# Optimization experiments

Measured on AMD Instinct MI355X. Metric: run time of the kernel, lower is better.

The kernel has to match this reference:

```python
import jax, jax.numpy as jnp
import numpy as np

BS, T, G, C = 64, 128, 36, 256
H = 256          # gaze LSTM hidden
P = 256          # spatial projected size
PT = 256         # temporal projected size
Q = 16           # queue size
NC = 10          # num classes
NEG = -1e9


def setup_inputs() -> dict:
    key = jax.random.key(0)
    ks = jax.random.split(key, 40)
    s = 0.02
    D = C + H
    inp = {
        'cnn_feat_seq': jax.random.normal(ks[0], (BS, T, G, C), jnp.float32),
        'gaze_seq': jax.random.normal(ks[1], (BS, T, 3), jnp.float32),
        # init-hidden / init-cell MLPs (Linear(3,H), Tanh, Linear(H,H), Tanh)
        'init_h_w1': jax.random.normal(ks[2], (H, 3)) * s, 'init_h_b1': jnp.zeros((H,)),
        'init_h_w2': jax.random.normal(ks[3], (H, H)) * s, 'init_h_b2': jnp.zeros((H,)),
        'init_c_w1': jax.random.normal(ks[4], (H, 3)) * s, 'init_c_b1': jnp.zeros((H,)),
        'init_c_w2': jax.random.normal(ks[5], (H, H)) * s, 'init_c_b2': jnp.zeros((H,)),
        # LSTM (input 3, hidden H), torch gate order i,f,g,o
        'lstm_wih': jax.random.normal(ks[6], (4 * H, 3)) * s, 'lstm_whh': jax.random.normal(ks[7], (4 * H, H)) * s,
        'lstm_bih': jnp.zeros((4 * H,)), 'lstm_bhh': jnp.zeros((4 * H,)),
        # spatial attention
        'sa_wl': jax.random.normal(ks[8], (P, H)) * s, 'sa_bl': jnp.zeros((P,)),
        'sa_wc': jax.random.normal(ks[9], (P, C)) * s, 'sa_bc': jnp.zeros((P,)),
        'sa_wz': jax.random.normal(ks[10], (P,)) * s,
        # temporal attention
        'ta_wl': jax.random.normal(ks[11], (PT, H)) * s, 'ta_bl': jnp.zeros((PT,)),
        'ta_wv': jax.random.normal(ks[12], (PT, C)) * s, 'ta_bv': jnp.zeros((PT,)),
        'ta_wz': jax.random.normal(ks[13], (PT,)) * s,
        # MLP classifier: Linear(D,D) -> Linear(D,D) -> Linear(D,NC), no nonlinearity
        'mlp_w1': jax.random.normal(ks[14], (D, D)) * s, 'mlp_b1': jnp.zeros((D,)),
        'mlp_w2': jax.random.normal(ks[15], (D, D)) * s, 'mlp_b2': jnp.zeros((D,)),
        'mlp_w3': jax.random.normal(ks[16], (NC, D)) * s, 'mlp_b3': jnp.zeros((NC,)),
    }
    return inp


def _forward(cnn_feat_seq, gaze_seq,
             init_h_w1, init_h_b1, init_h_w2, init_h_b2,
             init_c_w1, init_c_b1, init_c_w2, init_c_b2,
             lstm_wih, lstm_whh, lstm_bih, lstm_bhh,
             sa_wl, sa_bl, sa_wc, sa_bc, sa_wz,
             ta_wl, ta_bl, ta_wv, ta_bv, ta_wz,
             mlp_w1, mlp_b1, mlp_w2, mlp_b2, mlp_w3, mlp_b3):
    bs, num_frame = gaze_seq.shape[0], gaze_seq.shape[1]
    mean_gaze = jnp.mean(gaze_seq, axis=1)  # (bs, 3)
    # init MLP ends with Tanh, and forward applies F.tanh again
    h0 = jnp.tanh(jnp.tanh(jnp.tanh(mean_gaze @ init_h_w1.T + init_h_b1) @ init_h_w2.T + init_h_b2))
    c0 = jnp.tanh(jnp.tanh(jnp.tanh(mean_gaze @ init_c_w1.T + init_c_b1) @ init_c_w2.T + init_c_b2))
    buf_s0 = jnp.zeros((Q, bs, C), cnn_feat_seq.dtype)
    buf_h0 = jnp.zeros((Q, bs, H), cnn_feat_seq.dtype)
    qidx = jnp.arange(Q)

    def step(carry, xs):
        h, c, buf_s, buf_h, i = carry
        feat, gaze = xs  # (bs,G,C), (bs,3)
        # --- spatial additive attention over grids ---
        Hp = h @ sa_wl.T + sa_bl                                  # (bs,P)
        Vp = jnp.einsum('bgc,pc->bgp', feat, sa_wc) + sa_bc       # (bs,G,P)
        zs = jnp.tanh(Hp[:, None, :] + Vp) @ sa_wz                # (bs,G)
        sw = jax.nn.softmax(zs, axis=1)
        spat = jnp.einsum('bgc,bg->bc', feat, sw)                 # (bs,C)
        # --- rolling queues (newest last) ---
        buf_s = jnp.concatenate([buf_s[1:], spat[None]], axis=0)
        buf_h = jnp.concatenate([buf_h[1:], h[None]], axis=0)
        count = jnp.minimum(i + 1, Q)
        mask = qidx >= (Q - count)                                # (Q,) valid slots
        # --- temporal additive attention over queue ---
        Hq = jnp.einsum('qbh,ph->qbp', buf_h, ta_wl) + ta_bl
        Vq = jnp.einsum('qbc,pc->qbp', buf_s, ta_wv) + ta_bv
        zt = jnp.tanh(Hq + Vq) @ ta_wz                            # (Q,bs)
        zt = jnp.where(mask[:, None], zt, NEG)
        tw = jax.nn.softmax(zt, axis=0)
        temp = jnp.einsum('qbc,qb->bc', buf_s, tw)                # (bs,C)
        # --- one LSTM step on gaze ---
        gates = gaze @ lstm_wih.T + lstm_bih + h @ lstm_whh.T + lstm_bhh
        gi, gf, gg, go = jnp.split(gates, 4, axis=-1)
        c = jax.nn.sigmoid(gf) * c + jax.nn.sigmoid(gi) * jnp.tanh(gg)
        h = jax.nn.sigmoid(go) * jnp.tanh(c)
        # --- classifier on concat(temporal_feat, lstm_hidden) ---
        fc = jnp.concatenate([temp, h], axis=1)                   # (bs, C+H)
        pred = ((fc @ mlp_w1.T + mlp_b1) @ mlp_w2.T + mlp_b2) @ mlp_w3.T + mlp_b3
        return (h, c, buf_s, buf_h, i + 1), pred

    feats_t = jnp.swapaxes(cnn_feat_seq, 0, 1)  # (T,bs,G,C)
    gaze_t = jnp.swapaxes(gaze_seq, 0, 1)       # (T,bs,3)
    _, preds = jax.lax.scan(step, (h0, c0, buf_s0, buf_h0, jnp.int32(0)), (feats_t, gaze_t))
    # torch cats (1,bs,NC) pieces along dim=1 -> (1, T*bs, NC)
    return preds.reshape(1, num_frame * bs, NC)


def reference(cnn_feat_seq, gaze_seq,
              init_h_w1, init_h_b1, init_h_w2, init_h_b2,
              init_c_w1, init_c_b1, init_c_w2, init_c_b2,
              lstm_wih, lstm_whh, lstm_bih, lstm_bhh,
              sa_wl, sa_bl, sa_wc, sa_bc, sa_wz,
              ta_wl, ta_bl, ta_wv, ta_bv, ta_wz,
              mlp_w1, mlp_b1, mlp_w2, mlp_b2, mlp_w3, mlp_b3):
    return _forward(cnn_feat_seq, gaze_seq,
                    init_h_w1, init_h_b1, init_h_w2, init_h_b2,
                    init_c_w1, init_c_b1, init_c_w2, init_c_b2,
                    lstm_wih, lstm_whh, lstm_bih, lstm_bhh,
                    sa_wl, sa_bl, sa_wc, sa_bc, sa_wz,
                    ta_wl, ta_bl, ta_wv, ta_bv, ta_wz,
                    mlp_w1, mlp_b1, mlp_w2, mlp_b2, mlp_w3, mlp_b3)
```

## Files before the change

kernel.cpp:

```cpp
#include <hip/hip_runtime.h>
#include <cstdint>
#include <cstddef>

#define BSZ 64
#define TT  128
#define GG  36
#define CC  256
#define HH  256
#define QQ  16
#define NCLS 10
#define NROW 8192
#define SP_ROWS 32

using short8  = __attribute__((ext_vector_type(8))) short;
using f32x4   = __attribute__((ext_vector_type(4))) float;
using half2_t = __attribute__((ext_vector_type(2))) _Float16;
typedef unsigned int u32;
typedef unsigned short u16;

#define OFF_WI    0u
#define OFF_WF    131072u
#define OFF_WG    262144u
#define OFF_WO    393216u
#define OFF_SAWL  524288u
#define OFF_TAWL  655360u
#define OFF_TAWV  786432u
#define OFF_SAWC  917504u
#define OFF_W32   1048576u
#define OFF_WC    1069056u
#define OFF_BC    1089536u
#define OFF_H0F16 1089792u
#define OFF_C0    1122560u
#define OFF_HSEQ  1188096u
#define OFF_HSEQB 9642240u
#define OFF_HPSA  13869312u
#define OFF_HQ    22257920u
#define OFF_SPAT  30646528u
#define OFF_SPATB 39035136u
#define OFF_ZSC   43229440u
#define WS_NEEDED 43262208u

__device__ __forceinline__ float rcp_fast(float x){
#if __has_builtin(__builtin_amdgcn_rcpf)
  return __builtin_amdgcn_rcpf(x);
#else
  return 1.f/x;
#endif
}
__device__ __forceinline__ float fast_sig(float x){ return rcp_fast(1.f+__expf(-x)); }
__device__ __forceinline__ float fast_tanh(float x){ float e=__expf(2.f*x); return 1.f-2.f*rcp_fast(e+1.f); }
__device__ __forceinline__ u16 f2bf(float f){
  u32 u = __builtin_bit_cast(u32, f);
  u += 0x7fffu + ((u>>16)&1u);
  return (u16)(u>>16);
}
__device__ __forceinline__ float bf2f(u16 b){
  u32 u = ((u32)b)<<16; return __builtin_bit_cast(float, u);
}
__device__ __forceinline__ u32 cvtpk_bf16(float a, float b){
  u32 p;
  asm("v_cvt_pk_bf16_f32 %0, %1, %2" : "=v"(p) : "v"(a), "v"(b));
  return p;
}
__device__ __forceinline__ u32 packf16(float a, float b){
  half2_t h; h.x = (_Float16)a; h.y = (_Float16)b;
  return __builtin_bit_cast(u32, h);
}
__device__ __forceinline__ float dot2(u32 w, u32 h, float acc){
#if __has_builtin(__builtin_amdgcn_fdot2)
  return __builtin_amdgcn_fdot2(__builtin_bit_cast(half2_t, w),
                                __builtin_bit_cast(half2_t, h), acc, false);
#else
  half2_t a = __builtin_bit_cast(half2_t, w), b = __builtin_bit_cast(half2_t, h);
  return acc + (float)a.x*(float)b.x + (float)a.y*(float)b.y;
#endif
}
__device__ __forceinline__ f32x4 mfma16(short8 a, short8 b, f32x4 c){
  return __builtin_amdgcn_mfma_f32_16x16x32_bf16(a, b, c, 0, 0, 0);
}

__global__ void __launch_bounds__(256) k_prep1(const float* __restrict__ whh,
    const float* __restrict__ sawl, const float* __restrict__ tawl,
    const float* __restrict__ tawv, const float* __restrict__ sawc,
    const float* __restrict__ w3, const float* __restrict__ w2, char* ws){
  int blk = blockIdx.x, tid = threadIdx.x;
  if (blk < 512){
    u32* wq = (u32*)ws;
    for (int rr = 0; rr < 2; ++rr){
      int row = blk*2 + rr;
      float v  = whh[row*256 + tid];
      float vn = __shfl_down(v, 1);
      if ((tid & 1) == 0){
        int typ = row >> 8;
        int j   = row & 255;
        wq[typ*32768 + (tid>>1)*256 + j] = packf16(v, vn);
      }
    }
  } else if (blk < 544){
    int rel = blk - 512;
    int mat = rel >> 3;
    const float* src; u16* dst;
    if (mat==0){ src=sawl; dst=(u16*)(ws+OFF_SAWL); }
    else if (mat==1){ src=tawl; dst=(u16*)(ws+OFF_TAWL); }
    else if (mat==2){ src=tawv; dst=(u16*)(ws+OFF_TAWV); }
    else { src=sawc; dst=(u16*)(ws+OFF_SAWC); }
    int base = (rel & 7)*8192 + tid;
    if (mat < 3){
      for (int i = 0; i < 32; ++i){ int e = base + i*256; dst[e] = f2bf(src[e]); }
    } else {
      for (int i = 0; i < 32; ++i){
        int e = base + i*256;
        int col = e >> 8, kk = e & 255;
        dst[col*256 + (kk ^ ((col&7)<<3))] = f2bf(src[e]);
      }
    }
  } else {
    int idx = (blk-544)*256 + tid;
    int o = idx >> 9, k2 = idx & 511;
    float acc = 0.f;
    for (int m = 0; m < 512; ++m) acc = fmaf(w3[o*512+m], w2[m*512+k2], acc);
    ((float*)(ws+OFF_W32))[idx] = acc;
  }
}

__global__ void __launch_bounds__(256) k_prep2(const float* __restrict__ w1,
    const float* __restrict__ b1, const float* __restrict__ w3,
    const float* __restrict__ b2, const float* __restrict__ b3,
    const float* __restrict__ gaze,
    const float* __restrict__ ihw1, const float* __restrict__ ihb1,
    const float* __restrict__ ihw2, const float* __restrict__ ihb2,
    const float* __restrict__ icw1, const float* __restrict__ icb1,
    const float* __restrict__ icw2, const float* __restrict__ icb2,
    char* ws){
  int blk = blockIdx.x, tid = threadIdx.x;
  const float* W32 = (const float*)(ws+OFF_W32);
  if (blk < 20){
    int idx = blk*256 + tid; int o = idx>>9, k = idx&511;
    float acc = 0.f;
    for (int m = 0; m < 512; ++m) acc = fmaf(W32[o*512+m], w1[m*512+k], acc);
    ((float*)(ws+OFF_WC))[idx] = acc;
  } else if (blk == 20){
    if (tid < 10){
      float acc = b3[tid];
      for (int m = 0; m < 512; ++m) acc = fmaf(W32[tid*512+m], b1[m], acc);
      for (int m = 0; m < 512; ++m) acc = fmaf(w3[tid*512+m], b2[m], acc);
      ((float*)(ws+OFF_BC))[tid] = acc;
    }
  } else {
    int b = blk - 21;
    __shared__ float red0[128], red1[128], red2[128];
    __shared__ float mg[3];
    __shared__ float x1[256];
    if (tid < 128){
      const float* gp = gaze + b*384 + tid*3;
      red0[tid] = gp[0]; red1[tid] = gp[1]; red2[tid] = gp[2];
    }
    __syncthreads();
    for (int s = 64; s >= 1; s >>= 1){
      if (tid < s){ red0[tid]+=red0[tid+s]; red1[tid]+=red1[tid+s]; red2[tid]+=red2[tid+s]; }
      __syncthreads();
    }
    if (tid == 0){ mg[0]=red0[0]*(1.f/128.f); mg[1]=red1[0]*(1.f/128.f); mg[2]=red2[0]*(1.f/128.f); }
    __syncthreads();
    for (int which = 0; which < 2; ++which){
      const float* aw1 = which? icw1 : ihw1; const float* ab1 = which? icb1 : ihb1;
      const float* aw2 = which? icw2 : ihw2; const float* ab2 = which? icb2 : ihb2;
      float v = fast_tanh(fmaf(aw1[tid*3+2],mg[2], fmaf(aw1[tid*3+1],mg[1], fmaf(aw1[tid*3],mg[0], ab1[tid]))));
      x1[tid] = v;
      __syncthreads();
      float acc = ab2[tid];
      for (int k = 0; k < 256; ++k) acc = fmaf(aw2[tid*256+k], x1[k], acc);
      float h0 = fast_tanh(fast_tanh(acc));
      if (which == 0){
        float* hseq = (float*)(ws+OFF_HSEQ);
        hseq[(size_t)(0*64 + b)*256 + tid] = h0;
        float hn = __shfl_down(h0, 1);
        if ((tid&1)==0){
          ((u32*)(ws+OFF_HSEQB))[((size_t)(0*64+b)*256 + tid)>>1] = ((u32)f2bf(hn)<<16) | f2bf(h0);
          ((u32*)(ws+OFF_H0F16))[b*128 + (tid>>1)] = packf16(h0, hn);
        }
      } else {
        ((float*)(ws+OFF_C0))[b*256 + tid] = h0;
      }
      __syncthreads();
    }
  }
}

__global__ void __launch_bounds__(256) k_gates(const float* __restrict__ gaze,
    const float* __restrict__ wih, const float* __restrict__ bih,
    const float* __restrict__ bhh, char* ws){
  int b = blockIdx.x, tq = blockIdx.y, j = threadIdx.x;
  u32* pIG = (u32*)(ws+OFF_HPSA);
  u32* pFO = (u32*)(ws+OFF_HQ);
  float bi = bih[j]     + bhh[j];
  float bf_= bih[256+j] + bhh[256+j];
  float bg = bih[512+j] + bhh[512+j];
  float bo = bih[768+j] + bhh[768+j];
  float ui0=wih[j*3],       ui1=wih[j*3+1],       ui2=wih[j*3+2];
  float uf0=wih[(256+j)*3], uf1=wih[(256+j)*3+1], uf2=wih[(256+j)*3+2];
  float ug0=wih[(512+j)*3], ug1=wih[(512+j)*3+1], ug2=wih[(512+j)*3+2];
  float uo0=wih[(768+j)*3], uo1=wih[(768+j)*3+1], uo2=wih[(768+j)*3+2];
#pragma unroll
  for (int dt = 0; dt < 4; ++dt){
    int t = tq*4 + dt;
    float g0 = gaze[b*384 + t*3], g1 = gaze[b*384 + t*3 + 1], g2 = gaze[b*384 + t*3 + 2];
    float aI = fmaf(ui2,g2, fmaf(ui1,g1, fmaf(ui0,g0, bi)));
    float aF = fmaf(uf2,g2, fmaf(uf1,g1, fmaf(uf0,g0, bf_)));
    float aG = fmaf(ug2,g2, fmaf(ug1,g1, fmaf(ug0,g0, bg)));
    float aO = fmaf(uo2,g2, fmaf(uo1,g1, fmaf(uo0,g0, bo)));
    size_t idx = (size_t)(b*128 + t)*256 + j;
    pIG[idx] = packf16(aI, aG);
    pFO[idx] = packf16(aF, aO);
  }
}

__global__ void __launch_bounds__(512, 2) k_lstm(char* ws){
  int b = blockIdx.x, tid = threadIdx.x;
  int half = tid >> 8;
  int j = tid & 255;
  __shared__ __align__(16) uint4 lds_w4[4*512];
  __shared__ __align__(16) u32 hbuf[2][128];
  __shared__ float p_lds[256];

  const u32* wq = (const u32*)ws;
  const u32* wA = wq + (half ? 1 : 0) * 32768;
  const u32* wB = wq + (half ? 3 : 2) * 32768;
  u32 w0[128], w1r[112];
#pragma unroll
  for (int c = 0; c < 128; ++c) w0[c] = wA[c*256 + j];
#pragma unroll
  for (int c = 0; c < 112; ++c) w1r[c] = wB[c*256 + j];
#pragma unroll
  for (int cq = 0; cq < 4; ++cq){
    uint4 wv;
    wv.x = wB[(112 + cq*4 + 0)*256 + j];
    wv.y = wB[(112 + cq*4 + 1)*256 + j];
    wv.z = wB[(112 + cq*4 + 2)*256 + j];
    wv.w = wB[(112 + cq*4 + 3)*256 + j];
    lds_w4[cq*512 + tid] = wv;
  }
  if (tid < 128) hbuf[0][tid] = ((const u32*)(ws+OFF_H0F16))[b*128 + tid];
  float creg = half ? ((const float*)(ws+OFF_C0))[b*256 + j] : 0.f;

  const u32* gin = (const u32*)(ws + (half ? OFF_HQ : OFF_HPSA)) + (size_t)b*128*256 + j;
  float* hseq = (float*)(ws+OFF_HSEQ);
  u32* hseqb = (u32*)(ws+OFF_HSEQB);
  float hv_prev = 0.f; u32 hpk_prev = 0;
  u32 gcur = gin[0];
  __syncthreads();

  for (int t = 0; t < 128; ++t){
    int cur = t & 1, nxt = cur ^ 1;
    if (half == 1 && t > 0){
      hseq[((size_t)t*64 + b)*256 + j] = hv_prev;
      if ((j & 1) == 0)
        hseqb[(((size_t)t*64 + b)*256 + j)>>1] = hpk_prev;
    }
    u32 gnext = 0;
    if (t < 127) gnext = gin[(size_t)(t+1)*256];
    uint4 wp[4];
#pragma unroll
    for (int cq = 0; cq < 4; ++cq) wp[cq] = lds_w4[cq*512 + tid];

    half2_t gh = __builtin_bit_cast(half2_t, gcur);
    float aA0 = (float)gh.x, aA1 = 0.f;
    float aB0 = (float)gh.y, aB1 = 0.f;
#pragma unroll
    for (int c4 = 0; c4 < 28; ++c4){
      uint4 h4 = *reinterpret_cast<const uint4*>(&hbuf[cur][c4*4]);
      aA0 = dot2(w0[c4*4+0], h4.x, aA0); aB0 = dot2(w1r[c4*4+0], h4.x, aB0);
      aA1 = dot2(w0[c4*4+1], h4.y, aA1); aB1 = dot2(w1r[c4*4+1], h4.y, aB1);
      aA0 = dot2(w0[c4*4+2], h4.z, aA0); aB0 = dot2(w1r[c4*4+2], h4.z, aB0);
      aA1 = dot2(w0[c4*4+3], h4.w, aA1); aB1 = dot2(w1r[c4*4+3], h4.w, aB1);
    }
#pragma unroll
    for (int cq = 0; cq < 4; ++cq){
      int c4 = 28 + cq;
      uint4 h4 = *reinterpret_cast<const uint4*>(&hbuf[cur][c4*4]);
      uint4 wv = wp[cq];
      aA0 = dot2(w0[c4*4+0], h4.x, aA0); aB0 = dot2(wv.x, h4.x, aB0);
      aA1 = dot2(w0[c4*4+1], h4.y, aA1); aB1 = dot2(wv.y, h4.y, aB1);
      aA0 = dot2(w0[c4*4+2], h4.z, aA0); aB0 = dot2(wv.z, h4.z, aB0);
      aA1 = dot2(w0[c4*4+3], h4.w, aA1); aB1 = dot2(wv.w, h4.w, aB1);
    }
    float aA = aA0 + aA1, aB = aB0 + aB1;
    if (half == 0){
      p_lds[j] = fast_sig(aA) * fast_tanh(aB);
    }
    __syncthreads();
    if (half == 1){
      float p = p_lds[j];
      creg = fmaf(fast_sig(aA), creg, p);
      float hv = fast_sig(aB) * fast_tanh(creg);
      float hn = __shfl_down(hv, 1);
      if ((j & 1) == 0) hbuf[nxt][j>>1] = packf16(hv, hn);
      hv_prev = hv;
      hpk_prev = ((u32)f2bf(hn)<<16) | f2bf(hv);
    }
    __syncthreads();
    gcur = gnext;
  }
  if (half == 1){
    hseq[((size_t)128*64 + b)*256 + j] = hv_prev;
    if ((j & 1) == 0)
      hseqb[(((size_t)128*64 + b)*256 + j)>>1] = hpk_prev;
  }
}

__global__ void __launch_bounds__(256) k_proj1(const float* __restrict__ sabl,
    const float* __restrict__ sabc, const float* __restrict__ tabl,
    const float* __restrict__ tabv, char* ws){
  int bx = blockIdx.x, which = blockIdx.y;
  const u16* A = (const u16*)(ws+OFF_HSEQB);
  const u16* B = (const u16*)(ws + (which? OFF_TAWL : OFF_SAWL));
  float* Out   = (float*)(ws + (which? OFF_HQ : OFF_HPSA));
  const float* bp1 = which? tabl : sabl;
  const float* bp2 = which? tabv : sabc;
  int tid = threadIdx.x, w = tid>>6, l = tid&63;
  int lr = l&15, lk = l>>4;
  int rb = bx*64;
  short8 afr[4][8];
#pragma unroll
  for (int m = 0; m < 4; ++m)
#pragma unroll
    for (int k = 0; k < 8; ++k)
      afr[m][k] = *(const short8*)(const void*)(A + (size_t)(rb + m*16 + lr)*256 + k*32 + lk*8);
#pragma unroll
  for (int n = 0; n < 4; ++n){
    int cb = w*64 + n*16;
    int col = cb + lr;
    float bias = bp1[col] + bp2[col];
    f32x4 a0 = {0.f,0.f,0.f,0.f}, a1 = a0, a2 = a0, a3 = a0;
#pragma unroll
    for (int k = 0; k < 8; ++k){
      short8 bf = *(const short8*)(const void*)(B + (size_t)col*256 + k*32 + lk*8);
      a0 = mfma16(afr[0][k], bf, a0);
      a1 = mfma16(afr[1][k], bf, a1);
      a2 = mfma16(afr[2][k], bf, a2);
      a3 = mfma16(afr[3][k], bf, a3);
    }
#pragma unroll
    for (int q = 0; q < 4; ++q){
      Out[(size_t)(rb + 0*16 + lk*4 + q)*256 + col] = a0[q] + bias;
      Out[(size_t)(rb + 1*16 + lk*4 + q)*256 + col] = a1[q] + bias;
      Out[(size_t)(rb + 2*16 + lk*4 + q)*256 + col] = a2[q] + bias;
      Out[(size_t)(rb + 3*16 + lk*4 + q)*256 + col] = a3[q] + bias;
    }
  }
}

__global__ void __launch_bounds__(512, 2) k_spatial(const float* __restrict__ feat,
    const float* __restrict__ sawz, char* ws){
  __shared__ __align__(16) u16 featb[48*256];
  __shared__ __align__(16) float hp[256];
  __shared__ float wzs[256];
  __shared__ float zsbuf[8][48];
  __shared__ float swl[36];
  __shared__ float psum[2][256];
  int bx = blockIdx.x, tid = threadIdx.x, w = tid>>6, l = tid&63;
  int lr = l&15, lk = l>>4;
  int colbase = w*32;
  const float* hpsa = (const float*)(ws+OFF_HPSA);
  const u16* Bw = (const u16*)(ws+OFF_SAWC);

  short8 breg[2][8];
#pragma unroll
  for (int n = 0; n < 2; ++n){
    int col = colbase + n*16 + lr;
#pragma unroll
    for (int k = 0; k < 8; ++k)
      breg[n][k] = *(const short8*)(const void*)(Bw + (size_t)col*256 + ((k*32 + lk*8) ^ ((col&7)<<3)));
  }
  if (tid < 256) wzs[tid] = sawz[tid];

  float4 pf[5]; float4 ph;
  {
    int r0 = bx*SP_ROWS;
    int t = r0>>6, b = r0&63;
    const float4* fb = (const float4*)(feat + ((size_t)(b*128 + t))*9216);
#pragma unroll
    for (int ii = 0; ii < 4; ++ii) pf[ii] = fb[tid + ii*512];
    if (tid < 256) pf[4] = fb[2048 + tid];
    if (tid < 64) ph = ((const float4*)(hpsa + (size_t)r0*256))[tid];
  }
  __syncthreads();

  for (int i = 0; i < SP_ROWS; ++i){
    int r = bx*SP_ROWS + i;
#pragma unroll
    for (int ii = 0; ii < 4; ++ii){
      int e = tid + ii*512;
      int g = e >> 6, c4 = e & 63;
      uint2 pp;
      pp.x = cvtpk_bf16(pf[ii].x, pf[ii].y);
      pp.y = cvtpk_bf16(pf[ii].z, pf[ii].w);
      *reinterpret_cast<uint2*>((u32*)featb + g*128 + ((c4*2) ^ ((g&7)<<2))) = pp;
    }
    if (tid < 256){
      int e = 2048 + tid;
      int g = e >> 6, c4 = e & 63;
      uint2 pp;
      pp.x = cvtpk_bf16(pf[4].x, pf[4].y);
      pp.y = cvtpk_bf16(pf[4].z, pf[4].w);
      *reinterpret_cast<uint2*>((u32*)featb + g*128 + ((c4*2) ^ ((g&7)<<2))) = pp;
    }
    if (tid < 64) *reinterpret_cast<float4*>(hp + tid*4) = ph;
    __syncthreads();
    if (i + 1 < SP_ROWS){
      int rn = r + 1;
      int t = rn>>6, b = rn&63;
      const float4* fb = (const float4*)(feat + ((size_t)(b*128 + t))*9216);
#pragma unroll
      for (int ii = 0; ii < 4; ++ii) pf[ii] = fb[tid + ii*512];
      if (tid < 256) pf[4] = fb[2048 + tid];
      if (tid < 64) ph = ((const float4*)(hpsa + (size_t)rn*256))[tid];
    }
    float zacc[3][4] = {{0.f}};
#pragma unroll
    for (int m = 0; m < 3; ++m){
      short8 afr[8];
#pragma unroll
      for (int k = 0; k < 8; ++k){
        int g = m*16 + lr;
        afr[k] = *(const short8*)(const void*)(featb + g*256 + ((k*32 + lk*8) ^ ((g&7)<<3)));
      }
#pragma unroll
      for (int n = 0; n < 2; ++n){
        f32x4 a = {0.f,0.f,0.f,0.f};
#pragma unroll
        for (int k = 0; k < 8; ++k) a = mfma16(afr[k], breg[n][k], a);
        int col = colbase + n*16 + lr;
        float hpl = hp[col], wzv = wzs[col];
#pragma unroll
        for (int q = 0; q < 4; ++q)
          zacc[m][q] += fast_tanh(a[q] + hpl)*wzv;
      }
    }
#pragma unroll
    for (int m = 0; m < 3; ++m)
#pragma unroll
      for (int q = 0; q < 4; ++q){
        float v = zacc[m][q];
        v += __shfl_xor(v, 1); v += __shfl_xor(v, 2);
        v += __shfl_xor(v, 4); v += __shfl_xor(v, 8);
        if (lr == 0) zsbuf[w][m*16 + lk*4 + q] = v;
      }
    __syncthreads();
    if (w == 0){
      float z = -1e30f;
      if (l < 36)
        z = zsbuf[0][l]+zsbuf[1][l]+zsbuf[2][l]+zsbuf[3][l]
          + zsbuf[4][l]+zsbuf[5][l]+zsbuf[6][l]+zsbuf[7][l];
      float mx = z;
      for (int d = 1; d < 64; d <<= 1) mx = fmaxf(mx, __shfl_xor(mx, d));
      float e = (l < 36)? __expf(z - mx) : 0.f;
      float s = e;
      for (int d = 1; d < 64; d <<= 1) s += __shfl_xor(s, d);
      if (l < 36) swl[l] = e * rcp_fast(s);
    }
    __syncthreads();
    {
      int hsel = tid >> 8, col = tid & 255;
      float part = 0.f;
#pragma unroll
      for (int gg = 0; gg < 18; ++gg){
        int g = hsel*18 + gg;
        part = fmaf(swl[g], bf2f(featb[g*256 + (col ^ ((g&7)<<3))]), part);
      }
      psum[hsel][col] = part;
    }
    __syncthreads();
    if (tid < 256){
      float acc = psum[0][tid] + psum[1][tid];
      ((float*)(ws+OFF_SPAT))[(size_t)r*256 + tid] = acc;
      float an = __shfl_down(acc, 1);
      if ((tid & 1) == 0)
        ((u32*)(ws+OFF_SPATB))[((size_t)r*256 + tid)>>1] = cvtpk_bf16(acc, an);
    }
  }
}

__global__ void __launch_bounds__(256) k_proj2(const float* __restrict__ tawz, char* ws){
  int bx = blockIdx.x;
  int tid = threadIdx.x, w = tid>>6, l = tid&63;
  int lr = l&15, lk = l>>4;
  int rb = bx*64;
  const u16* A = (const u16*)(ws+OFF_SPATB);
  const u16* B = (const u16*)(ws+OFF_TAWV);
  const float* Hq = (const float*)(ws+OFF_HQ);
  __shared__ float zbuf[4][64];
  short8 afr[4][8];
#pragma unroll
  for (int m = 0; m < 4; ++m)
#pragma unroll
    for (int k = 0; k < 8; ++k)
      afr[m][k] = *(const short8*)(const void*)(A + (size_t)(rb + m*16 + lr)*256 + k*32 + lk*8);
  float racc[4][4] = {{0.f}};
#pragma unroll
  for (int n = 0; n < 4; ++n){
    int col = w*64 + n*16 + lr;
    float tzl = tawz[col];
    f32x4 a0 = {0.f,0.f,0.f,0.f}, a1 = a0, a2 = a0, a3 = a0;
#pragma unroll
    for (int k = 0; k < 8; ++k){
      short8 bf = *(const short8*)(const void*)(B + (size_t)col*256 + k*32 + lk*8);
      a0 = mfma16(afr[0][k], bf, a0);
      a1 = mfma16(afr[1][k], bf, a1);
      a2 = mfma16(afr[2][k], bf, a2);
      a3 = mfma16(afr[3][k], bf, a3);
    }
#pragma unroll
    for (int q = 0; q < 4; ++q){
      racc[0][q] += fast_tanh(a0[q] + Hq[(size_t)(rb + 0*16 + lk*4 + q)*256 + col]) * tzl;
      racc[1][q] += fast_tanh(a1[q] + Hq[(size_t)(rb + 1*16 + lk*4 + q)*256 + col]) * tzl;
      racc[2][q] += fast_tanh(a2[q] + Hq[(size_t)(rb + 2*16 + lk*4 + q)*256 + col]) * tzl;
      racc[3][q] += fast_tanh(a3[q] + Hq[(size_t)(rb + 3*16 + lk*4 + q)*256 + col]) * tzl;
    }
  }
#pragma unroll
  for (int m = 0; m < 4; ++m)
#pragma unroll
    for (int q = 0; q < 4; ++q){
      float v = racc[m][q];
      v += __shfl_xor(v, 1); v += __shfl_xor(v, 2);
      v += __shfl_xor(v, 4); v += __shfl_xor(v, 8);
      if (lr == 0) zbuf[w][m*16 + lk*4 + q] = v;
    }
  __syncthreads();
  if (tid < 64)
    ((float*)(ws+OFF_ZSC))[rb + tid] = zbuf[0][tid]+zbuf[1][tid]+zbuf[2][tid]+zbuf[3][tid];
}

__global__ void __launch_bounds__(256) k_final(float* __restrict__ out, char* ws){
  int bx = blockIdx.x;
  int b = bx & 63, tb = bx >> 6;
  int t0 = tb*8;
  int tid = threadIdx.x;
  int wv = tid>>6, l = tid&63;
  __shared__ float spw[23][256];
  __shared__ float zw[23];
  __shared__ float WcL[5120];
  __shared__ float bcL[10];
  __shared__ float w16[16];
  __shared__ float wpart[4][10];
  const float* spat = (const float*)(ws+OFF_SPAT);
  const float* zsc  = (const float*)(ws+OFF_ZSC);
  const float* hseq = (const float*)(ws+OFF_HSEQ);
  const float* Wc   = (const float*)(ws+OFF_WC);
#pragma unroll
  for (int i = 0; i < 20; ++i) WcL[tid + i*256] = Wc[tid + i*256];
  if (tid < 10) bcL[tid] = ((const float*)(ws+OFF_BC))[tid];
  for (int i = 0; i < 23; ++i){
    int tau = t0 - 15 + i;
    spw[i][tid] = (tau >= 0)? spat[(size_t)(tau*64 + b)*256 + tid] : 0.f;
  }
  if (tid < 23){
    int tau = t0 - 15 + tid;
    zw[tid] = (tau >= 0)? zsc[tau*64 + b] : -1e9f;
  }
  __syncthreads();
  for (int dt = 0; dt < 8; ++dt){
    int t = t0 + dt;
    if (wv == 0 && l < 16){
      float z = zw[dt + l];
      float mx = z;
      mx = fmaxf(mx, __shfl_xor(mx,1)); mx = fmaxf(mx, __shfl_xor(mx,2));
      mx = fmaxf(mx, __shfl_xor(mx,4)); mx = fmaxf(mx, __shfl_xor(mx,8));
      float e = __expf(z - mx);
      float s = e;
      s += __shfl_xor(s,1); s += __shfl_xor(s,2); s += __shfl_xor(s,4); s += __shfl_xor(s,8);
      w16[l] = e / s;
    }
    __syncthreads();
    float temp = 0.f;
#pragma unroll
    for (int qi = 0; qi < 16; ++qi) temp = fmaf(w16[qi], spw[dt+qi][tid], temp);
    float hc = hseq[(size_t)((t+1)*64 + b)*256 + tid];
    float po[10];
#pragma unroll
    for (int o = 0; o < 10; ++o){
      float v = fmaf(temp, WcL[o*512 + tid], hc*WcL[o*512 + 256 + tid]);
      v += __shfl_xor(v,1);  v += __shfl_xor(v,2);  v += __shfl_xor(v,4);
      v += __shfl_xor(v,8);  v += __shfl_xor(v,16); v += __shfl_xor(v,32);
      po[o] = v;
    }
    if (l == 0){
#pragma unroll
      for (int o = 0; o < 10; ++o) wpart[wv][o] = po[o];
    }
    __syncthreads();
    if (tid < 10)
      out[(size_t)(t*64 + b)*10 + tid] = wpart[0][tid]+wpart[1][tid]+wpart[2][tid]+wpart[3][tid] + bcL[tid];
    __syncthreads();
  }
}

extern "C" void kernel_launch(void* const* d_in, const int* in_sizes, int n_in,
                              void* d_out, int out_size, void* d_ws, size_t ws_size,
                              hipStream_t stream){
  const float* feat = (const float*)d_in[0];
  const float* gaze = (const float*)d_in[1];
  const float* ihw1 = (const float*)d_in[2];  const float* ihb1 = (const float*)d_in[3];
  const float* ihw2 = (const float*)d_in[4];  const float* ihb2 = (const float*)d_in[5];
  const float* icw1 = (const float*)d_in[6];  const float* icb1 = (const float*)d_in[7];
  const float* icw2 = (const float*)d_in[8];  const float* icb2 = (const float*)d_in[9];
  const float* wih  = (const float*)d_in[10]; const float* whh  = (const float*)d_in[11];
  const float* bih  = (const float*)d_in[12]; const float* bhh  = (const float*)d_in[13];
  const float* sawl = (const float*)d_in[14]; const float* sabl = (const float*)d_in[15];
  const float* sawc = (const float*)d_in[16]; const float* sabc = (const float*)d_in[17];
  const float* sawz = (const float*)d_in[18];
  const float* tawl = (const float*)d_in[19]; const float* tabl = (const float*)d_in[20];
  const float* tawv = (const float*)d_in[21]; const float* tabv = (const float*)d_in[22];
  const float* tawz = (const float*)d_in[23];
  const float* w1 = (const float*)d_in[24]; const float* b1 = (const float*)d_in[25];
  const float* w2 = (const float*)d_in[26]; const float* b2 = (const float*)d_in[27];
  const float* w3 = (const float*)d_in[28]; const float* b3 = (const float*)d_in[29];
  char* ws = (char*)d_ws;
  float* out = (float*)d_out;
  if (ws_size < (size_t)WS_NEEDED) return;

  k_prep1<<<dim3(564), dim3(256), 0, stream>>>(whh, sawl, tawl, tawv, sawc, w3, w2, ws);
  k_prep2<<<dim3(85), dim3(256), 0, stream>>>(w1, b1, w3, b2, b3, gaze,
      ihw1, ihb1, ihw2, ihb2, icw1, icb1, icw2, icb2, ws);
  k_gates<<<dim3(64, 32), dim3(256), 0, stream>>>(gaze, wih, bih, bhh, ws);
  k_lstm<<<dim3(64), dim3(512), 0, stream>>>(ws);
  k_proj1<<<dim3(128, 2), dim3(256), 0, stream>>>(sabl, sabc, tabl, tabv, ws);
  k_spatial<<<dim3(256), dim3(512), 0, stream>>>(feat, sawz, ws);
  k_proj2<<<dim3(128), dim3(256), 0, stream>>>(tawz, ws);
  k_final<<<dim3(1024), dim3(256), 0, stream>>>(out, ws);
}
```

Measured before the change: 610.0 us.

## Fuse input-gate projection into LSTM kernel and broadcast hidden state via readlane

Drops the separate gate precompute kernel and computes the gaze input projection inside the recurrent LSTM loop, with gaze staged in LDS. The per-step hidden vector is read once per lane and broadcast with readlane instead of repeated LDS vector loads. Fewer weights stay in registers (64 instead of 112) and more are moved to a larger LDS buffer. This cuts a kernel launch and the global traffic for the precomputed gates, and may lower register pressure. The cost is extra LDS weight reads inside the serial recurrence and a 128 KB LDS allocation, which limits occupancy.

```diff
diff --git a/kernel.cpp b/kernel.cpp
--- a/kernel.cpp
+++ b/kernel.cpp
@@ -187,67 +187,46 @@
   }
 }
 
-__global__ void __launch_bounds__(256) k_gates(const float* __restrict__ gaze,
+__global__ void __launch_bounds__(512, 2) k_lstm(const float* __restrict__ gaze,
     const float* __restrict__ wih, const float* __restrict__ bih,
     const float* __restrict__ bhh, char* ws){
-  int b = blockIdx.x, tq = blockIdx.y, j = threadIdx.x;
-  u32* pIG = (u32*)(ws+OFF_HPSA);
-  u32* pFO = (u32*)(ws+OFF_HQ);
-  float bi = bih[j]     + bhh[j];
-  float bf_= bih[256+j] + bhh[256+j];
-  float bg = bih[512+j] + bhh[512+j];
-  float bo = bih[768+j] + bhh[768+j];
-  float ui0=wih[j*3],       ui1=wih[j*3+1],       ui2=wih[j*3+2];
-  float uf0=wih[(256+j)*3], uf1=wih[(256+j)*3+1], uf2=wih[(256+j)*3+2];
-  float ug0=wih[(512+j)*3], ug1=wih[(512+j)*3+1], ug2=wih[(512+j)*3+2];
-  float uo0=wih[(768+j)*3], uo1=wih[(768+j)*3+1], uo2=wih[(768+j)*3+2];
-#pragma unroll
-  for (int dt = 0; dt < 4; ++dt){
-    int t = tq*4 + dt;
-    float g0 = gaze[b*384 + t*3], g1 = gaze[b*384 + t*3 + 1], g2 = gaze[b*384 + t*3 + 2];
-    float aI = fmaf(ui2,g2, fmaf(ui1,g1, fmaf(ui0,g0, bi)));
-    float aF = fmaf(uf2,g2, fmaf(uf1,g1, fmaf(uf0,g0, bf_)));
-    float aG = fmaf(ug2,g2, fmaf(ug1,g1, fmaf(ug0,g0, bg)));
-    float aO = fmaf(uo2,g2, fmaf(uo1,g1, fmaf(uo0,g0, bo)));
-    size_t idx = (size_t)(b*128 + t)*256 + j;
-    pIG[idx] = packf16(aI, aG);
-    pFO[idx] = packf16(aF, aO);
-  }
-}
-
-__global__ void __launch_bounds__(512, 2) k_lstm(char* ws){
   int b = blockIdx.x, tid = threadIdx.x;
   int half = tid >> 8;
   int j = tid & 255;
-  __shared__ __align__(16) uint4 lds_w4[4*512];
+  int l = tid & 63;
+  __shared__ u32 lds_w[16*2048];
   __shared__ __align__(16) u32 hbuf[2][128];
   __shared__ float p_lds[256];
+  __shared__ float g_lds[384];
 
   const u32* wq = (const u32*)ws;
   const u32* wA = wq + (half ? 1 : 0) * 32768;
   const u32* wB = wq + (half ? 3 : 2) * 32768;
-  u32 w0[128], w1r[112];
+  u32 w0[128], w1r[64];
 #pragma unroll
   for (int c = 0; c < 128; ++c) w0[c] = wA[c*256 + j];
 #pragma unroll
-  for (int c = 0; c < 112; ++c) w1r[c] = wB[c*256 + j];
-#pragma unroll
-  for (int cq = 0; cq < 4; ++cq){
-    uint4 wv;
-    wv.x = wB[(112 + cq*4 + 0)*256 + j];
-    wv.y = wB[(112 + cq*4 + 1)*256 + j];
-    wv.z = wB[(112 + cq*4 + 2)*256 + j];
-    wv.w = wB[(112 + cq*4 + 3)*256 + j];
-    lds_w4[cq*512 + tid] = wv;
-  }
+  for (int c = 0; c < 64; ++c)  w1r[c] = wB[c*256 + j];
+#pragma unroll
+  for (int cq = 0; cq < 16; ++cq)
+#pragma unroll
+    for (int q = 0; q < 4; ++q)
+      lds_w[cq*2048 + tid*4 + q] = wB[(64 + cq*4 + q)*256 + j];
+
+  if (tid < 384) g_lds[tid] = gaze[b*384 + tid];
   if (tid < 128) hbuf[0][tid] = ((const u32*)(ws+OFF_H0F16))[b*128 + tid];
   float creg = half ? ((const float*)(ws+OFF_C0))[b*256 + j] : 0.f;
 
-  const u32* gin = (const u32*)(ws + (half ? OFF_HQ : OFF_HPSA)) + (size_t)b*128*256 + j;
+  int rA = half ? 256 + j : j;
+  int rB = half ? 768 + j : 512 + j;
+  float baseA = bih[rA] + bhh[rA];
+  float baseB = bih[rB] + bhh[rB];
+  float uA0 = wih[rA*3], uA1 = wih[rA*3+1], uA2 = wih[rA*3+2];
+  float uB0 = wih[rB*3], uB1 = wih[rB*3+1], uB2 = wih[rB*3+2];
+
   float* hseq = (float*)(ws+OFF_HSEQ);
   u32* hseqb = (u32*)(ws+OFF_HSEQB);
   float hv_prev = 0.f; u32 hpk_prev = 0;
-  u32 gcur = gin[0];
   __syncthreads();
 
   for (int t = 0; t < 128; ++t){
@@ -257,32 +236,28 @@
       if ((j & 1) == 0)
         hseqb[(((size_t)t*64 + b)*256 + j)>>1] = hpk_prev;
     }
-    u32 gnext = 0;
-    if (t < 127) gnext = gin[(size_t)(t+1)*256];
-    uint4 wp[4];
-#pragma unroll
-    for (int cq = 0; cq < 4; ++cq) wp[cq] = lds_w4[cq*512 + tid];
-
-    half2_t gh = __builtin_bit_cast(half2_t, gcur);
-    float aA0 = (float)gh.x, aA1 = 0.f;
-    float aB0 = (float)gh.y, aB1 = 0.f;
-#pragma unroll
-    for (int c4 = 0; c4 < 28; ++c4){
-      uint4 h4 = *reinterpret_cast<const uint4*>(&hbuf[cur][c4*4]);
-      aA0 = dot2(w0[c4*4+0], h4.x, aA0); aB0 = dot2(w1r[c4*4+0], h4.x, aB0);
-      aA1 = dot2(w0[c4*4+1], h4.y, aA1); aB1 = dot2(w1r[c4*4+1], h4.y, aB1);
-      aA0 = dot2(w0[c4*4+2], h4.z, aA0); aB0 = dot2(w1r[c4*4+2], h4.z, aB0);
-      aA1 = dot2(w0[c4*4+3], h4.w, aA1); aB1 = dot2(w1r[c4*4+3], h4.w, aB1);
-    }
-#pragma unroll
-    for (int cq = 0; cq < 4; ++cq){
-      int c4 = 28 + cq;
-      uint4 h4 = *reinterpret_cast<const uint4*>(&hbuf[cur][c4*4]);
-      uint4 wv = wp[cq];
-      aA0 = dot2(w0[c4*4+0], h4.x, aA0); aB0 = dot2(wv.x, h4.x, aB0);
-      aA1 = dot2(w0[c4*4+1], h4.y, aA1); aB1 = dot2(wv.y, h4.y, aB1);
-      aA0 = dot2(w0[c4*4+2], h4.z, aA0); aB0 = dot2(wv.z, h4.z, aB0);
-      aA1 = dot2(w0[c4*4+3], h4.w, aA1); aB1 = dot2(wv.w, h4.w, aB1);
+    float g0 = g_lds[t*3], g1 = g_lds[t*3+1], g2 = g_lds[t*3+2];
+    float aA0 = fmaf(uA2,g2, fmaf(uA1,g1, fmaf(uA0,g0, baseA))), aA1 = 0.f;
+    float aB0 = fmaf(uB2,g2, fmaf(uB1,g1, fmaf(uB0,g0, baseB))), aB1 = 0.f;
+    uint2 hsl = *reinterpret_cast<const uint2*>(&hbuf[cur][l*2]);
+    int hs0 = (int)hsl.x, hs1 = (int)hsl.y;
+#pragma unroll
+    for (int c4 = 0; c4 < 32; ++c4){
+      u32 hx = (u32)__builtin_amdgcn_readlane(hs0, 2*c4);
+      u32 hy = (u32)__builtin_amdgcn_readlane(hs1, 2*c4);
+      u32 hz = (u32)__builtin_amdgcn_readlane(hs0, 2*c4 + 1);
+      u32 hw = (u32)__builtin_amdgcn_readlane(hs1, 2*c4 + 1);
+      u32 wb0, wb1, wb2, wb3;
+      if (c4 < 16){
+        wb0 = w1r[c4*4]; wb1 = w1r[c4*4+1]; wb2 = w1r[c4*4+2]; wb3 = w1r[c4*4+3];
+      } else {
+        uint4 wv = *reinterpret_cast<const uint4*>(&lds_w[(c4-16)*2048 + tid*4]);
+        wb0 = wv.x; wb1 = wv.y; wb2 = wv.z; wb3 = wv.w;
+      }
+      aA0 = dot2(w0[c4*4+0], hx, aA0); aB0 = dot2(wb0, hx, aB0);
+      aA1 = dot2(w0[c4*4+1], hy, aA1); aB1 = dot2(wb1, hy, aB1);
+      aA0 = dot2(w0[c4*4+2], hz, aA0); aB0 = dot2(wb2, hz, aB0);
+      aA1 = dot2(w0[c4*4+3], hw, aA1); aB1 = dot2(wb3, hw, aB1);
     }
     float aA = aA0 + aA1, aB = aB0 + aB1;
     if (half == 0){
@@ -299,7 +274,6 @@
       hpk_prev = ((u32)f2bf(hn)<<16) | f2bf(hv);
     }
     __syncthreads();
-    gcur = gnext;
   }
   if (half == 1){
     hseq[((size_t)128*64 + b)*256 + j] = hv_prev;
@@ -623,8 +597,7 @@
   k_prep1<<<dim3(564), dim3(256), 0, stream>>>(whh, sawl, tawl, tawv, sawc, w3, w2, ws);
   k_prep2<<<dim3(85), dim3(256), 0, stream>>>(w1, b1, w3, b2, b3, gaze,
       ihw1, ihb1, ihw2, ihb2, icw1, icb1, icw2, icb2, ws);
-  k_gates<<<dim3(64, 32), dim3(256), 0, stream>>>(gaze, wih, bih, bhh, ws);
-  k_lstm<<<dim3(64), dim3(512), 0, stream>>>(ws);
+  k_lstm<<<dim3(64), dim3(512), 0, stream>>>(gaze, wih, bih, bhh, ws);
   k_proj1<<<dim3(128, 2), dim3(256), 0, stream>>>(sabl, sabc, tabl, tabv, ws);
   k_spatial<<<dim3(256), dim3(512), 0, stream>>>(feat, sawz, ws);
   k_proj2<<<dim3(128), dim3(256), 0, stream>>>(tawz, ws);
```

Result: faster. 527.5 us (-13.5%).
